# Performance work log

Hardware: AMD Instinct MI355X
Metric: run time of the kernel (lower is better)

## Reference

```python
import jax, jax.numpy as jnp
import numpy as np

N_NODES = 50000
N_EDGES = 800000
N_FEAT = 128
DIM = 32
N_GRAPHS = 500
N_CLASSES = 2


def setup_inputs() -> dict:
    key = jax.random.key(0)
    ks = jax.random.split(key, 10)
    x = jax.random.normal(ks[0], (N_NODES, N_FEAT), dtype=jnp.float32)
    edge_index = jax.random.randint(ks[1], (2, N_EDGES), 0, N_NODES, dtype=jnp.int64)
    batch = jnp.sort(jax.random.randint(ks[2], (N_NODES,), 0, N_GRAPHS, dtype=jnp.int64))
    edge_weight = jax.random.uniform(ks[3], (N_EDGES,), dtype=jnp.float32)
    s = 1.0 / np.sqrt(N_FEAT)
    w_rel = jax.random.uniform(ks[4], (N_FEAT, DIM), jnp.float32, -s, s)
    b_rel = jax.random.uniform(ks[5], (DIM,), jnp.float32, -s, s)
    w_root = jax.random.uniform(ks[6], (N_FEAT, DIM), jnp.float32, -s, s)
    s2 = 1.0 / np.sqrt(DIM)
    w_fc1 = jax.random.uniform(ks[7], (DIM, DIM), jnp.float32, -s2, s2)
    b_fc1 = jnp.zeros((DIM,), jnp.float32)
    w_fc2 = jax.random.uniform(ks[8], (DIM, N_CLASSES), jnp.float32, -s2, s2)
    b_fc2 = jnp.zeros((N_CLASSES,), jnp.float32)
    return {"x": x, "edge_weight": edge_weight, "w_rel": w_rel, "b_rel": b_rel,
            "w_root": w_root, "w_fc1": w_fc1, "b_fc1": b_fc1, "w_fc2": w_fc2,
            "b_fc2": b_fc2, "edge_index": edge_index, "batch": batch}


def reference(x, edge_weight, w_rel, b_rel, w_root, w_fc1, b_fc1, w_fc2, b_fc2,
              edge_index, batch):
    src, dst = edge_index[0], edge_index[1]
    # GraphConv: out_i = lin_rel(sum_{j->i} w_ji * x_j) + lin_root(x_i)
    msg = x[src] * edge_weight[:, None]                      # [E, F]
    agg = jax.ops.segment_sum(msg, dst, num_segments=N_NODES)  # [N, F]
    h = agg @ w_rel + b_rel + x @ w_root                     # [N, DIM]
    h = jax.nn.relu(h)
    # global_add_pool over graph ids
    pooled = jax.ops.segment_sum(h, batch, num_segments=N_GRAPHS)  # [G, DIM]
    h2 = jax.nn.relu(pooled @ w_fc1 + b_fc1)
    # dropout is identity in eval mode
    logits = h2 @ w_fc2 + b_fc2
    return jax.nn.log_softmax(logits, axis=-1)
```

## Files before the change

kernel.cpp:

```cpp
#include <hip/hip_runtime.h>

#define NN 50000
#define NE 800000
#define NF 128
#define DIM 32
#define NG 500
#define BK 32
#define NB ((NN + BK - 1) / BK)
#define PB 782
#define HB 128
#define CHUNK_E ((NE + HB - 1) / HB)
#define CAP 1024
#define SC7 7

__device__ __forceinline__ unsigned rne16(float f) {
    unsigned u = __float_as_uint(f);
    return (u + 0x7FFFu + ((u >> 16) & 1u)) >> 16;
}
#define UIF __uint_as_float
__device__ __forceinline__ float blo(unsigned p) { return UIF(p << 16); }
__device__ __forceinline__ float bhi(unsigned p) { return UIF(p & 0xFFFF0000u); }

__global__ __launch_bounds__(256) void projhist_kernel(
    const float* __restrict__ x, const float* __restrict__ w_rel,
    const float* __restrict__ w_root, const float* __restrict__ b_rel,
    unsigned* __restrict__ yp, unsigned* __restrict__ rootp,
    const int* __restrict__ ei, int* __restrict__ H, float* __restrict__ pooled)
{
    __shared__ float s_w[2 * NF * DIM];
    int tid = threadIdx.x;

    if (blockIdx.x >= PB) {
        int blk = blockIdx.x - PB;
        int* sh = (int*)s_w;
        int pi = blk * 256 + tid;
        if (pi < NG * DIM) pooled[pi] = 0.0f;
        for (int i = tid; i < NB; i += 256) sh[i] = 0;
        __syncthreads();
        int base = blk * CHUNK_E;
        int end  = min(base + CHUNK_E, NE);
        for (int e = base + tid; e < end; e += 256)
            atomicAdd(&sh[ei[NE + e] >> 5], 1);
        __syncthreads();
        for (int i = tid; i < NB; i += 256) H[blk * NB + i] = sh[i];
        return;
    }

    {
        const float4* wr4 = reinterpret_cast<const float4*>(w_rel);
        const float4* wo4 = reinterpret_cast<const float4*>(w_root);
        float4* s4 = reinterpret_cast<float4*>(s_w);
#pragma unroll
        for (int j = 0; j < 4; ++j) s4[tid + j * 256]        = wr4[tid + j * 256];
#pragma unroll
        for (int j = 0; j < 4; ++j) s4[1024 + tid + j * 256] = wo4[tid + j * 256];
    }

    int cg_ = tid & 15;
    int rg  = tid >> 4;
    int c0  = cg_ * 4;
    int rb  = blockIdx.x * 64 + rg * 4;

    const float* Wb = (c0 < DIM) ? (s_w + c0) : (s_w + NF * DIM + (c0 - DIM));

    int r0s = min(rb + 0, NN - 1);
    int r1s = min(rb + 1, NN - 1);
    int r2s = min(rb + 2, NN - 1);
    int r3s = min(rb + 3, NN - 1);
    const float* x0 = x + (size_t)r0s * NF;
    const float* x1 = x + (size_t)r1s * NF;
    const float* x2 = x + (size_t)r2s * NF;
    const float* x3 = x + (size_t)r3s * NF;

    __syncthreads();

    float4 a0 = {0,0,0,0}, a1 = {0,0,0,0}, a2 = {0,0,0,0}, a3 = {0,0,0,0};

#define F4FMA(acc, xv, wa, wb_, wc, wd)                                \
    acc.x = fmaf(xv.x, wa.x, acc.x);  acc.y = fmaf(xv.x, wa.y, acc.y); \
    acc.z = fmaf(xv.x, wa.z, acc.z);  acc.w = fmaf(xv.x, wa.w, acc.w); \
    acc.x = fmaf(xv.y, wb_.x, acc.x); acc.y = fmaf(xv.y, wb_.y, acc.y); \
    acc.z = fmaf(xv.y, wb_.z, acc.z); acc.w = fmaf(xv.y, wb_.w, acc.w); \
    acc.x = fmaf(xv.z, wc.x, acc.x);  acc.y = fmaf(xv.z, wc.y, acc.y); \
    acc.z = fmaf(xv.z, wc.z, acc.z);  acc.w = fmaf(xv.z, wc.w, acc.w); \
    acc.x = fmaf(xv.w, wd.x, acc.x);  acc.y = fmaf(xv.w, wd.y, acc.y); \
    acc.z = fmaf(xv.w, wd.z, acc.z);  acc.w = fmaf(xv.w, wd.w, acc.w)

    float4 na = *reinterpret_cast<const float4*>(x0);
    float4 nb = *reinterpret_cast<const float4*>(x1);
    float4 nc = *reinterpret_cast<const float4*>(x2);
    float4 nd = *reinterpret_cast<const float4*>(x3);
#pragma unroll
    for (int k = 0; k < NF; k += 4) {
        float4 xa = na, xb = nb, xc = nc, xd = nd;
        if (k + 4 < NF) {
            na = *reinterpret_cast<const float4*>(x0 + k + 4);
            nb = *reinterpret_cast<const float4*>(x1 + k + 4);
            nc = *reinterpret_cast<const float4*>(x2 + k + 4);
            nd = *reinterpret_cast<const float4*>(x3 + k + 4);
        }
        float4 wa  = *reinterpret_cast<const float4*>(Wb + (k + 0) * DIM);
        float4 wb2 = *reinterpret_cast<const float4*>(Wb + (k + 1) * DIM);
        float4 wc  = *reinterpret_cast<const float4*>(Wb + (k + 2) * DIM);
        float4 wd  = *reinterpret_cast<const float4*>(Wb + (k + 3) * DIM);
        F4FMA(a0, xa, wa, wb2, wc, wd);
        F4FMA(a1, xb, wa, wb2, wc, wd);
        F4FMA(a2, xc, wa, wb2, wc, wd);
        F4FMA(a3, xd, wa, wb2, wc, wd);
    }
#undef F4FMA

#define PACK2(v) make_uint2(rne16(v.x) | (rne16(v.y) << 16), rne16(v.z) | (rne16(v.w) << 16))
    if (c0 < DIM) {
        int cp0 = c0 >> 1;
        if (rb + 0 < NN) *reinterpret_cast<uint2*>(yp + (size_t)(rb+0) * 16 + cp0) = PACK2(a0);
        if (rb + 1 < NN) *reinterpret_cast<uint2*>(yp + (size_t)(rb+1) * 16 + cp0) = PACK2(a1);
        if (rb + 2 < NN) *reinterpret_cast<uint2*>(yp + (size_t)(rb+2) * 16 + cp0) = PACK2(a2);
        if (rb + 3 < NN) *reinterpret_cast<uint2*>(yp + (size_t)(rb+3) * 16 + cp0) = PACK2(a3);
    } else {
        int cc  = c0 - DIM;
        int cp0 = cc >> 1;
        float4 bi = *reinterpret_cast<const float4*>(b_rel + cc);
        a0.x += bi.x; a0.y += bi.y; a0.z += bi.z; a0.w += bi.w;
        a1.x += bi.x; a1.y += bi.y; a1.z += bi.z; a1.w += bi.w;
        a2.x += bi.x; a2.y += bi.y; a2.z += bi.z; a2.w += bi.w;
        a3.x += bi.x; a3.y += bi.y; a3.z += bi.z; a3.w += bi.w;
        if (rb + 0 < NN) *reinterpret_cast<uint2*>(rootp + (size_t)(rb+0) * 16 + cp0) = PACK2(a0);
        if (rb + 1 < NN) *reinterpret_cast<uint2*>(rootp + (size_t)(rb+1) * 16 + cp0) = PACK2(a1);
        if (rb + 2 < NN) *reinterpret_cast<uint2*>(rootp + (size_t)(rb+2) * 16 + cp0) = PACK2(a2);
        if (rb + 3 < NN) *reinterpret_cast<uint2*>(rootp + (size_t)(rb+3) * 16 + cp0) = PACK2(a3);
    }
#undef PACK2
}

__global__ __launch_bounds__(256) void colscan(
    int* __restrict__ H, int* __restrict__ colsum)
{
    int b = blockIdx.x * 256 + threadIdx.x;
    if (b >= NB) return;
    int run = 0;
#pragma unroll 8
    for (int blk = 0; blk < HB; ++blk) {
        int v = H[blk * NB + b];
        H[blk * NB + b] = run;
        run += v;
    }
    colsum[b] = run;
}

__global__ __launch_bounds__(256) void partition_kernel(
    const int* __restrict__ ei, const float* __restrict__ ew,
    const int* __restrict__ H, const int* __restrict__ colsum,
    uint2* __restrict__ part, int* __restrict__ boff)
{
    __shared__ int s_scan[256];
    __shared__ int s_boff[NB + 1];
    __shared__ int cur[NB];
    int t = threadIdx.x;
    {
        int v[SC7]; int sum = 0;
#pragma unroll
        for (int j = 0; j < SC7; ++j) {
            int idx = t * SC7 + j;
            v[j] = (idx < NB) ? colsum[idx] : 0;
            sum += v[j];
        }
        s_scan[t] = sum;
        __syncthreads();
        for (int o = 1; o < 256; o <<= 1) {
            int u = (t >= o) ? s_scan[t - o] : 0;
            __syncthreads();
            s_scan[t] += u;
            __syncthreads();
        }
        int b2 = s_scan[t] - sum;
#pragma unroll
        for (int j = 0; j < SC7; ++j) {
            int idx = t * SC7 + j;
            if (idx < NB) { s_boff[idx] = b2; b2 += v[j]; }
        }
        if (t == 0) s_boff[NB] = NE;
        __syncthreads();
    }
    if (blockIdx.x == 0)
        for (int i = t; i <= NB; i += 256) boff[i] = s_boff[i];

    for (int i = t; i < NB; i += 256)
        cur[i] = s_boff[i] + H[blockIdx.x * NB + i];
    __syncthreads();
    int base = blockIdx.x * CHUNK_E;
    int end  = min(base + CHUNK_E, NE);
    for (int e = base + t; e < end; e += 256) {
        int s = ei[e], d = ei[NE + e];
        float w = ew[e];
        int b = d >> 5;
        int pos = atomicAdd(&cur[b], 1);
        part[pos] = make_uint2((unsigned)s | ((unsigned)(d & 31) << 16),
                               __float_as_uint(w));
    }
}

__global__ __launch_bounds__(256) void bucketagg_kernel(
    const uint2* __restrict__ ypq, const uint2* __restrict__ rootq,
    const uint2* __restrict__ part, const int* __restrict__ boff,
    const int* __restrict__ batch, float* __restrict__ pooled)
{
    __shared__ unsigned csr_lds[CAP];
    __shared__ int cnt[BK];
    __shared__ int cur[BK];
    __shared__ int off[BK + 1];
    int b = blockIdx.x, t = threadIdx.x;
    int s0 = boff[b], s1 = boff[b + 1], m = s1 - s0;

    uint2 rec[4];
    int nrec = 0;
    if (t < BK) cnt[t] = 0;
    __syncthreads();
#pragma unroll
    for (int i = 0; i < 4; ++i) {
        int idx = t + i * 256;
        if (idx < m) { rec[i] = part[s0 + idx]; nrec = i + 1; }
    }
#pragma unroll
    for (int i = 0; i < 4; ++i)
        if (i < nrec) atomicAdd(&cnt[rec[i].x >> 16], 1);
    __syncthreads();
    if (t < BK) {
        int v = cnt[t];
        int inc = v;
#pragma unroll
        for (int o = 1; o < BK; o <<= 1) {
            int u = __shfl_up(inc, o, 64);
            if (t >= o) inc += u;
        }
        off[t] = inc - v;
        cur[t] = inc - v;
        if (t == BK - 1) off[BK] = inc;
    }
    __syncthreads();
#pragma unroll
    for (int i = 0; i < 4; ++i)
        if (i < nrec) {
            uint2 pk = rec[i];
            int nl = pk.x >> 16;
            int pos = atomicAdd(&cur[nl], 1);
            csr_lds[pos] = (pk.x & 0xFFFFu) | (rne16(UIF(pk.y)) << 16);
        }
    if (t < BK) {
        int n = b * BK + t;
        cnt[t] = (n < NN) ? batch[n] : -1;
    }
    __syncthreads();

    int w    = t >> 6;
    int lane = t & 63;
    int g    = lane >> 3;
    int j    = lane & 7;
    int nl   = w * 8 + g;
    int n    = b * BK + nl;
    float v0 = 0, v1 = 0, v2 = 0, v3 = 0;
    if (n < NN) {
        int e  = off[nl];
        int e1 = off[nl + 1];
        for (; e + 4 <= e1; e += 4) {
            unsigned c0 = csr_lds[e],     c1 = csr_lds[e + 1];
            unsigned c2 = csr_lds[e + 2], c3 = csr_lds[e + 3];
            uint2 p0 = ypq[(c0 & 0xFFFFu) * 8 + j];
            uint2 p1 = ypq[(c1 & 0xFFFFu) * 8 + j];
            uint2 p2 = ypq[(c2 & 0xFFFFu) * 8 + j];
            uint2 p3 = ypq[(c3 & 0xFFFFu) * 8 + j];
            float w0 = UIF(c0 & 0xFFFF0000u), w1 = UIF(c1 & 0xFFFF0000u);
            float w2 = UIF(c2 & 0xFFFF0000u), w3 = UIF(c3 & 0xFFFF0000u);
            v0 = fmaf(w0, blo(p0.x), v0); v1 = fmaf(w0, bhi(p0.x), v1);
            v2 = fmaf(w0, blo(p0.y), v2); v3 = fmaf(w0, bhi(p0.y), v3);
            v0 = fmaf(w1, blo(p1.x), v0); v1 = fmaf(w1, bhi(p1.x), v1);
            v2 = fmaf(w1, blo(p1.y), v2); v3 = fmaf(w1, bhi(p1.y), v3);
            v0 = fmaf(w2, blo(p2.x), v0); v1 = fmaf(w2, bhi(p2.x), v1);
            v2 = fmaf(w2, blo(p2.y), v2); v3 = fmaf(w2, bhi(p2.y), v3);
            v0 = fmaf(w3, blo(p3.x), v0); v1 = fmaf(w3, bhi(p3.x), v1);
            v2 = fmaf(w3, blo(p3.y), v2); v3 = fmaf(w3, bhi(p3.y), v3);
        }
        for (; e < e1; ++e) {
            unsigned cu = csr_lds[e];
            uint2 p = ypq[(cu & 0xFFFFu) * 8 + j];
            float ww = UIF(cu & 0xFFFF0000u);
            v0 = fmaf(ww, blo(p.x), v0); v1 = fmaf(ww, bhi(p.x), v1);
            v2 = fmaf(ww, blo(p.y), v2); v3 = fmaf(ww, bhi(p.y), v3);
        }
        uint2 rr = rootq[(size_t)n * 8 + j];
        v0 = fmaxf(v0 + blo(rr.x), 0.0f);
        v1 = fmaxf(v1 + bhi(rr.x), 0.0f);
        v2 = fmaxf(v2 + blo(rr.y), 0.0f);
        v3 = fmaxf(v3 + bhi(rr.y), 0.0f);
    }
    __syncthreads();

    float* s_p = (float*)csr_lds;
    {
        float* dst = s_p + nl * DIM + 4 * j;
        dst[0] = v0; dst[1] = v1; dst[2] = v2; dst[3] = v3;
    }
    __syncthreads();

    int gi = t >> 5, c = t & 31;
    int rung = -1; float run = 0.0f;
#pragma unroll
    for (int k = 0; k < 4; ++k) {
        int nl2 = gi * 4 + k;
        int n2  = b * BK + nl2;
        if (n2 >= NN) break;
        float v = s_p[nl2 * DIM + c];
        int gg = cnt[nl2];
        if (gg != rung) {
            if (rung >= 0) atomicAdd(&pooled[rung * DIM + c], run);
            rung = gg; run = v;
        } else run += v;
    }
    if (rung >= 0) atomicAdd(&pooled[rung * DIM + c], run);
}

__global__ __launch_bounds__(512) void head_kernel(
    const float* __restrict__ pooled, const float* __restrict__ w_fc1,
    const float* __restrict__ b_fc1, const float* __restrict__ w_fc2,
    const float* __restrict__ b_fc2, float* __restrict__ out)
{
    __shared__ float s_fc1[DIM * DIM];
    __shared__ float s_b1[DIM];
    __shared__ float s_fc2[DIM * 2];
    __shared__ float s_b2[2];
    int tid = threadIdx.x;
    s_fc1[tid]       = w_fc1[tid];
    s_fc1[tid + 512] = w_fc1[tid + 512];
    if (tid < DIM * 2) s_fc2[tid] = w_fc2[tid];
    if (tid < DIM)     s_b1[tid]  = b_fc1[tid];
    if (tid < 2)       s_b2[tid]  = b_fc2[tid];
    __syncthreads();

    int g = tid;
    if (g >= NG) return;
    const float* p = pooled + g * DIM;
    float h2[DIM];
#pragma unroll
    for (int c = 0; c < DIM; ++c) {
        float a = s_b1[c];
#pragma unroll
        for (int k = 0; k < DIM; ++k)
            a = fmaf(p[k], s_fc1[k * DIM + c], a);
        h2[c] = a > 0.0f ? a : 0.0f;
    }
    float l0 = s_b2[0], l1 = s_b2[1];
#pragma unroll
    for (int c = 0; c < DIM; ++c) {
        l0 = fmaf(h2[c], s_fc2[c * 2 + 0], l0);
        l1 = fmaf(h2[c], s_fc2[c * 2 + 1], l1);
    }
    float m   = fmaxf(l0, l1);
    float lse = m + logf(expf(l0 - m) + expf(l1 - m));
    out[g * 2 + 0] = l0 - lse;
    out[g * 2 + 1] = l1 - lse;
}

extern "C" void kernel_launch(void* const* d_in, const int* in_sizes, int n_in,
                              void* d_out, int out_size, void* d_ws, size_t ws_size,
                              hipStream_t stream) {
    const float* x      = (const float*)d_in[0];
    const float* ew     = (const float*)d_in[1];
    const float* w_rel  = (const float*)d_in[2];
    const float* b_rel  = (const float*)d_in[3];
    const float* w_root = (const float*)d_in[4];
    const float* w_fc1  = (const float*)d_in[5];
    const float* b_fc1  = (const float*)d_in[6];
    const float* w_fc2  = (const float*)d_in[7];
    const float* b_fc2  = (const float*)d_in[8];
    const int*   ei     = (const int*)d_in[9];
    const int*   batch  = (const int*)d_in[10];
    float* out = (float*)d_out;

    char* ws = (char*)d_ws;
    unsigned* yp    = (unsigned*)ws;
    unsigned* rootp = yp + (size_t)NN * 16;
    uint2* part     = (uint2*)(rootp + (size_t)NN * 16);
    int*   H        = (int*)(part + NE);
    int*   colsum   = H + (size_t)HB * NB;
    int*   boff     = colsum + NB;
    float* pooled   = (float*)(boff + NB + 2);

    projhist_kernel<<<PB + HB, 256, 0, stream>>>(x, w_rel, w_root, b_rel,
                                                 yp, rootp, ei, H, pooled);
    colscan<<<(NB + 255) / 256, 256, 0, stream>>>(H, colsum);
    partition_kernel<<<HB, 256, 0, stream>>>(ei, ew, H, colsum, part, boff);
    bucketagg_kernel<<<NB, 256, 0, stream>>>((const uint2*)yp, (const uint2*)rootp,
                                             part, boff, batch, pooled);
    head_kernel<<<1, 512, 0, stream>>>(pooled, w_fc1, b_fc1, w_fc2, b_fc2, out);
}
```

Measured before the change: 75.53 us.

## Compute node projections with bf16 MFMA instead of scalar FP32 FMAs

Replaces the scalar FP32 FMA projection of x against w_rel and w_root with bf16 MFMA 16x16x32 instructions. The weights are stored transposed as bf16 in padded shared memory, and each wave converts its x rows to bf16. Results are staged through a padded shared buffer so the packed bf16 stores to yp and rootp stay coalesced. This cuts ALU work in the projection, but the inputs are now rounded to bf16 before the multiply, which adds precision error, and shared-memory usage goes up.

```diff
diff --git a/kernel.cpp b/kernel.cpp
--- a/kernel.cpp
+++ b/kernel.cpp
@@ -13,6 +13,10 @@
 #define CAP 1024
 #define SC7 7
 
+typedef float  f32x4  __attribute__((ext_vector_type(4)));
+typedef __bf16 bf16x8 __attribute__((ext_vector_type(8)));
+typedef unsigned short u16x8 __attribute__((ext_vector_type(8)));
+
 __device__ __forceinline__ unsigned rne16(float f) {
     unsigned u = __float_as_uint(f);
     return (u + 0x7FFFu + ((u >> 16) & 1u)) >> 16;
@@ -27,12 +31,13 @@
     unsigned* __restrict__ yp, unsigned* __restrict__ rootp,
     const int* __restrict__ ei, int* __restrict__ H, float* __restrict__ pooled)
 {
-    __shared__ float s_w[2 * NF * DIM];
+    __shared__ unsigned short s_wb[64 * 136];
+    __shared__ float s_out[64 * 65];
     int tid = threadIdx.x;
 
     if (blockIdx.x >= PB) {
         int blk = blockIdx.x - PB;
-        int* sh = (int*)s_w;
+        int* sh = (int*)s_wb;
         int pi = blk * 256 + tid;
         if (pi < NG * DIM) pooled[pi] = 0.0f;
         for (int i = tid; i < NB; i += 256) sh[i] = 0;
@@ -46,91 +51,73 @@
         return;
     }
 
-    {
-        const float4* wr4 = reinterpret_cast<const float4*>(w_rel);
-        const float4* wo4 = reinterpret_cast<const float4*>(w_root);
-        float4* s4 = reinterpret_cast<float4*>(s_w);
-#pragma unroll
-        for (int j = 0; j < 4; ++j) s4[tid + j * 256]        = wr4[tid + j * 256];
-#pragma unroll
-        for (int j = 0; j < 4; ++j) s4[1024 + tid + j * 256] = wo4[tid + j * 256];
-    }
-
-    int cg_ = tid & 15;
-    int rg  = tid >> 4;
-    int c0  = cg_ * 4;
-    int rb  = blockIdx.x * 64 + rg * 4;
-
-    const float* Wb = (c0 < DIM) ? (s_w + c0) : (s_w + NF * DIM + (c0 - DIM));
-
-    int r0s = min(rb + 0, NN - 1);
-    int r1s = min(rb + 1, NN - 1);
-    int r2s = min(rb + 2, NN - 1);
-    int r3s = min(rb + 3, NN - 1);
-    const float* x0 = x + (size_t)r0s * NF;
-    const float* x1 = x + (size_t)r1s * NF;
-    const float* x2 = x + (size_t)r2s * NF;
-    const float* x3 = x + (size_t)r3s * NF;
-
-    __syncthreads();
-
-    float4 a0 = {0,0,0,0}, a1 = {0,0,0,0}, a2 = {0,0,0,0}, a3 = {0,0,0,0};
-
-#define F4FMA(acc, xv, wa, wb_, wc, wd)                                \
-    acc.x = fmaf(xv.x, wa.x, acc.x);  acc.y = fmaf(xv.x, wa.y, acc.y); \
-    acc.z = fmaf(xv.x, wa.z, acc.z);  acc.w = fmaf(xv.x, wa.w, acc.w); \
-    acc.x = fmaf(xv.y, wb_.x, acc.x); acc.y = fmaf(xv.y, wb_.y, acc.y); \
-    acc.z = fmaf(xv.y, wb_.z, acc.z); acc.w = fmaf(xv.y, wb_.w, acc.w); \
-    acc.x = fmaf(xv.z, wc.x, acc.x);  acc.y = fmaf(xv.z, wc.y, acc.y); \
-    acc.z = fmaf(xv.z, wc.z, acc.z);  acc.w = fmaf(xv.z, wc.w, acc.w); \
-    acc.x = fmaf(xv.w, wd.x, acc.x);  acc.y = fmaf(xv.w, wd.y, acc.y); \
-    acc.z = fmaf(xv.w, wd.z, acc.z);  acc.w = fmaf(xv.w, wd.w, acc.w)
-
-    float4 na = *reinterpret_cast<const float4*>(x0);
-    float4 nb = *reinterpret_cast<const float4*>(x1);
-    float4 nc = *reinterpret_cast<const float4*>(x2);
-    float4 nd = *reinterpret_cast<const float4*>(x3);
-#pragma unroll
-    for (int k = 0; k < NF; k += 4) {
-        float4 xa = na, xb = nb, xc = nc, xd = nd;
-        if (k + 4 < NF) {
-            na = *reinterpret_cast<const float4*>(x0 + k + 4);
-            nb = *reinterpret_cast<const float4*>(x1 + k + 4);
-            nc = *reinterpret_cast<const float4*>(x2 + k + 4);
-            nd = *reinterpret_cast<const float4*>(x3 + k + 4);
-        }
-        float4 wa  = *reinterpret_cast<const float4*>(Wb + (k + 0) * DIM);
-        float4 wb2 = *reinterpret_cast<const float4*>(Wb + (k + 1) * DIM);
-        float4 wc  = *reinterpret_cast<const float4*>(Wb + (k + 2) * DIM);
-        float4 wd  = *reinterpret_cast<const float4*>(Wb + (k + 3) * DIM);
-        F4FMA(a0, xa, wa, wb2, wc, wd);
-        F4FMA(a1, xb, wa, wb2, wc, wd);
-        F4FMA(a2, xc, wa, wb2, wc, wd);
-        F4FMA(a3, xd, wa, wb2, wc, wd);
-    }
-#undef F4FMA
-
-#define PACK2(v) make_uint2(rne16(v.x) | (rne16(v.y) << 16), rne16(v.z) | (rne16(v.w) << 16))
-    if (c0 < DIM) {
-        int cp0 = c0 >> 1;
-        if (rb + 0 < NN) *reinterpret_cast<uint2*>(yp + (size_t)(rb+0) * 16 + cp0) = PACK2(a0);
-        if (rb + 1 < NN) *reinterpret_cast<uint2*>(yp + (size_t)(rb+1) * 16 + cp0) = PACK2(a1);
-        if (rb + 2 < NN) *reinterpret_cast<uint2*>(yp + (size_t)(rb+2) * 16 + cp0) = PACK2(a2);
-        if (rb + 3 < NN) *reinterpret_cast<uint2*>(yp + (size_t)(rb+3) * 16 + cp0) = PACK2(a3);
-    } else {
-        int cc  = c0 - DIM;
-        int cp0 = cc >> 1;
-        float4 bi = *reinterpret_cast<const float4*>(b_rel + cc);
-        a0.x += bi.x; a0.y += bi.y; a0.z += bi.z; a0.w += bi.w;
-        a1.x += bi.x; a1.y += bi.y; a1.z += bi.z; a1.w += bi.w;
-        a2.x += bi.x; a2.y += bi.y; a2.z += bi.z; a2.w += bi.w;
-        a3.x += bi.x; a3.y += bi.y; a3.z += bi.z; a3.w += bi.w;
-        if (rb + 0 < NN) *reinterpret_cast<uint2*>(rootp + (size_t)(rb+0) * 16 + cp0) = PACK2(a0);
-        if (rb + 1 < NN) *reinterpret_cast<uint2*>(rootp + (size_t)(rb+1) * 16 + cp0) = PACK2(a1);
-        if (rb + 2 < NN) *reinterpret_cast<uint2*>(rootp + (size_t)(rb+2) * 16 + cp0) = PACK2(a2);
-        if (rb + 3 < NN) *reinterpret_cast<uint2*>(rootp + (size_t)(rb+3) * 16 + cp0) = PACK2(a3);
-    }
-#undef PACK2
+    for (int i = tid; i < 64 * NF; i += 256) {
+        int k   = i >> 6;
+        int col = i & 63;
+        float v = (col < DIM) ? w_rel[k * DIM + col] : w_root[k * DIM + (col - DIM)];
+        s_wb[col * 136 + k] = (unsigned short)rne16(v);
+    }
+    int rb = blockIdx.x * 64;
+    __syncthreads();
+
+    int l    = tid & 63;
+    int w    = tid >> 6;
+    int mrow = l & 15;
+    int q    = l >> 4;
+    int arow = min(rb + w * 16 + mrow, NN - 1);
+    const float* xr = x + (size_t)arow * NF + q * 8;
+
+    f32x4 acc0 = {0,0,0,0}, acc1 = {0,0,0,0}, acc2 = {0,0,0,0}, acc3 = {0,0,0,0};
+#pragma unroll
+    for (int k0 = 0; k0 < NF; k0 += 32) {
+        float4 xa = *reinterpret_cast<const float4*>(xr + k0);
+        float4 xb = *reinterpret_cast<const float4*>(xr + k0 + 4);
+        u16x8 au;
+        au[0] = (unsigned short)rne16(xa.x); au[1] = (unsigned short)rne16(xa.y);
+        au[2] = (unsigned short)rne16(xa.z); au[3] = (unsigned short)rne16(xa.w);
+        au[4] = (unsigned short)rne16(xb.x); au[5] = (unsigned short)rne16(xb.y);
+        au[6] = (unsigned short)rne16(xb.z); au[7] = (unsigned short)rne16(xb.w);
+        bf16x8 a = __builtin_bit_cast(bf16x8, au);
+        int kb = k0 + q * 8;
+        bf16x8 b0 = *reinterpret_cast<const bf16x8*>(&s_wb[(0  + mrow) * 136 + kb]);
+        bf16x8 b1 = *reinterpret_cast<const bf16x8*>(&s_wb[(16 + mrow) * 136 + kb]);
+        bf16x8 b2 = *reinterpret_cast<const bf16x8*>(&s_wb[(32 + mrow) * 136 + kb]);
+        bf16x8 b3 = *reinterpret_cast<const bf16x8*>(&s_wb[(48 + mrow) * 136 + kb]);
+        acc0 = __builtin_amdgcn_mfma_f32_16x16x32_bf16(a, b0, acc0, 0, 0, 0);
+        acc1 = __builtin_amdgcn_mfma_f32_16x16x32_bf16(a, b1, acc1, 0, 0, 0);
+        acc2 = __builtin_amdgcn_mfma_f32_16x16x32_bf16(a, b2, acc2, 0, 0, 0);
+        acc3 = __builtin_amdgcn_mfma_f32_16x16x32_bf16(a, b3, acc3, 0, 0, 0);
+    }
+#pragma unroll
+    for (int reg = 0; reg < 4; ++reg) {
+        int srow = w * 16 + q * 4 + reg;
+        s_out[srow * 65 +  0 + mrow] = acc0[reg];
+        s_out[srow * 65 + 16 + mrow] = acc1[reg];
+        s_out[srow * 65 + 32 + mrow] = acc2[reg];
+        s_out[srow * 65 + 48 + mrow] = acc3[reg];
+    }
+    __syncthreads();
+
+#pragma unroll
+    for (int rep = 0; rep < 8; ++rep) {
+        int idx = tid + rep * 256;
+        int row = idx >> 5;
+        int ui  = idx & 31;
+        int n   = rb + row;
+        if (n < NN) {
+            if (ui < 16) {
+                int c0 = ui * 2;
+                unsigned p = rne16(s_out[row * 65 + c0]) |
+                             (rne16(s_out[row * 65 + c0 + 1]) << 16);
+                yp[(size_t)n * 16 + ui] = p;
+            } else {
+                int c0 = (ui - 16) * 2;
+                float f0 = s_out[row * 65 + DIM + c0]     + b_rel[c0];
+                float f1 = s_out[row * 65 + DIM + c0 + 1] + b_rel[c0 + 1];
+                rootp[(size_t)n * 16 + (ui - 16)] = rne16(f0) | (rne16(f1) << 16);
+            }
+        }
+    }
 }
 
 __global__ __launch_bounds__(256) void colscan(
```

Result: faster. 66.99 us (-11.3%).
